# Kernel optimization log

Hardware: AMD Instinct MI355X
Metric: run time of the kernel (lower is better)

The kernel has to match this reference:

```python
import jax, jax.numpy as jnp
import numpy as np

D_MODEL = 1024
N_LAYERS = 4
D_INNER = 2 * D_MODEL          # expand=2
D_STATE = 16
D_CONV = 4
DT_RANK = D_MODEL // 16        # ceil(1024/16)=64
B, T = 2, 1024


def setup_inputs() -> dict:
    key = jax.random.key(0)
    ks = jax.random.split(key, 8)
    s = 0.02
    return {
        "x": jax.random.normal(ks[0], (B, T, D_MODEL), jnp.float32),
        "in_proj_w": jax.random.normal(ks[1], (N_LAYERS, 2 * D_INNER, D_MODEL), jnp.float32) * s,
        "conv_w": jax.random.normal(ks[2], (N_LAYERS, D_INNER, D_CONV), jnp.float32) * s,
        "conv_b": jnp.zeros((N_LAYERS, D_INNER), jnp.float32),
        "x_proj_w": jax.random.normal(ks[3], (N_LAYERS, DT_RANK + 2 * D_STATE, D_INNER), jnp.float32) * s,
        "dt_proj_w": jax.random.normal(ks[4], (N_LAYERS, D_INNER, DT_RANK), jnp.float32) * s,
        "dt_proj_b": jax.random.normal(ks[5], (N_LAYERS, D_INNER), jnp.float32) * 0.1,
        "A_log": jnp.tile(jnp.log(jnp.arange(1.0, D_STATE + 1.0, dtype=jnp.float32)), (N_LAYERS, D_INNER, 1)),
        "Dd": jnp.ones((N_LAYERS, D_INNER), jnp.float32),
        "out_proj_w": jax.random.normal(ks[6], (N_LAYERS, D_MODEL, D_INNER), jnp.float32) * s,
        "norm_w": jnp.ones((D_MODEL,), jnp.float32),
        "norm_b": jnp.zeros((D_MODEL,), jnp.float32),
    }


def _silu(v):
    return v * jax.nn.sigmoid(v)


def _mamba_block(x, in_w, cw, cb, xp_w, dtp_w, dtp_b, A_log, Dv, out_w):
    # x: [B,T,d_model]
    xz = jnp.einsum('btd,ed->bte', x, in_w)            # [B,T,2*d_inner]
    u, z = jnp.split(xz, 2, axis=-1)                   # each [B,T,d_inner]
    # causal depthwise conv over time
    uc = jax.lax.conv_general_dilated(
        u.transpose(0, 2, 1),                          # [B,d_inner,T]
        cw[:, None, :],                                # [d_inner,1,K]
        window_strides=(1,), padding=[(D_CONV - 1, 0)],
        feature_group_count=D_INNER,
        dimension_numbers=('NCH', 'OIH', 'NCH'))
    uc = _silu(uc.transpose(0, 2, 1) + cb)             # [B,T,d_inner]
    x_dbl = jnp.einsum('btd,ed->bte', uc, xp_w)        # [B,T,dt_rank+2*d_state]
    dt_r = x_dbl[..., :DT_RANK]
    Bm = x_dbl[..., DT_RANK:DT_RANK + D_STATE]         # [B,T,d_state]
    Cm = x_dbl[..., DT_RANK + D_STATE:]                # [B,T,d_state]
    dt = jax.nn.softplus(jnp.einsum('btr,dr->btd', dt_r, dtp_w) + dtp_b)  # [B,T,d_inner]
    A = -jnp.exp(A_log)                                # [d_inner,d_state]

    def step(h, inp):
        u_t, dt_t, B_t, C_t = inp                      # [B,dI],[B,dI],[B,dS],[B,dS]
        h = jnp.exp(dt_t[..., None] * A) * h + (dt_t * u_t)[..., None] * B_t[:, None, :]
        return h, jnp.einsum('bds,bs->bd', h, C_t)

    h0 = jnp.zeros((x.shape[0], D_INNER, D_STATE), x.dtype)
    xs = (uc.transpose(1, 0, 2), dt.transpose(1, 0, 2), Bm.transpose(1, 0, 2), Cm.transpose(1, 0, 2))
    _, ys = jax.lax.scan(step, h0, xs)                 # ys: [T,B,d_inner]
    y = ys.transpose(1, 0, 2) + uc * Dv                # skip term D*u
    y = y * _silu(z)                                   # gated
    return jnp.einsum('btd,ed->bte', y, out_w)         # [B,T,d_model]


def reference(x, in_proj_w, conv_w, conv_b, x_proj_w, dt_proj_w, dt_proj_b, A_log, Dd, out_proj_w, norm_w, norm_b):
    for i in range(in_proj_w.shape[0]):
        residual = x
        x = _mamba_block(x, in_proj_w[i], conv_w[i], conv_b[i], x_proj_w[i],
                         dt_proj_w[i], dt_proj_b[i], A_log[i], Dd[i], out_proj_w[i])
        x = x + residual
    mu = jnp.mean(x, -1, keepdims=True)
    var = jnp.var(x, -1, keepdims=True)
    return (x - mu) / jnp.sqrt(var + 1e-5) * norm_w + norm_b
```

## Files before the change

### kernel.cpp

```cpp
#include <hip/hip_runtime.h>
#include <hip/hip_bf16.h>

#define N_LAYERS 4
#define D_MODEL  1024
#define D_INNER  2048
#define D_STATE  16
#define D_CONV   4
#define DT_RANK  64
#define BB       2
#define TT       1024
#define BT       (BB*TT)

#define NCHUNK 16
#define SCTC   (TT/NCHUNK)

#define XP_KS  8

typedef unsigned short ushort_t;
typedef __attribute__((ext_vector_type(8))) short short8;
typedef __attribute__((ext_vector_type(4))) float f32x4;

__device__ __forceinline__ float sigmoidf_(float x){ return 1.f/(1.f+__expf(-x)); }
__device__ __forceinline__ float siluf_(float x){ return x*sigmoidf_(x); }
__device__ __forceinline__ float softplusf_(float x){ return fmaxf(x,0.f) + log1pf(__expf(-fabsf(x))); }
__device__ __forceinline__ ushort_t f2b(float f){
    unsigned int x = __builtin_bit_cast(unsigned int, f);
    unsigned int r = (x + 0x7fffu + ((x>>16)&1u)) >> 16;
    return (ushort_t)r;
}
__device__ __forceinline__ float b2f(ushort_t u){
    unsigned int x = ((unsigned int)u) << 16;
    return __builtin_bit_cast(float, x);
}

#define GLOAD(g, l) __builtin_amdgcn_global_load_lds( \
    (const __attribute__((address_space(1))) void*)(g), \
    (__attribute__((address_space(3))) void*)(l), 16, 0, 0)

__global__ __launch_bounds__(256) void f2b_k(const float* __restrict__ in,
                                             ushort_t* __restrict__ out, int n){
    int i = blockIdx.x*256 + threadIdx.x;
    float4 v = ((const float4*)in)[i];
    ushort4 o;
    o.x = f2b(v.x); o.y = f2b(v.y); o.z = f2b(v.z); o.w = f2b(v.w);
    ((ushort4*)out)[i] = o;
}

__global__ __launch_bounds__(256) void f2b2_k(
    const float* __restrict__ a, ushort_t* __restrict__ ao, int na4,
    const float* __restrict__ b, ushort_t* __restrict__ bo){
    int i = blockIdx.x*256 + threadIdx.x;
    const float4* src; ushort4* dst; int j;
    if (i < na4){ src = (const float4*)a; dst = (ushort4*)ao; j = i; }
    else        { src = (const float4*)b; dst = (ushort4*)bo; j = i - na4; }
    float4 v = src[j];
    ushort4 o;
    o.x = f2b(v.x); o.y = f2b(v.y); o.z = f2b(v.z); o.w = f2b(v.w);
    dst[j] = o;
}

__global__ __launch_bounds__(512) void gemm_ip(
    const ushort_t* __restrict__ A, const ushort_t* __restrict__ W,
    int M, int N, int K, ushort_t* __restrict__ outb,
    int RM, int RN, int XN)
{
    __shared__ ushort_t As[4][128*32];
    __shared__ ushort_t Ws[4][128*32];
    const int tid  = threadIdx.x;
    const int lane = tid & 63;
    const int wv   = tid >> 6;
    const int wm0  = (wv>>2)*64, wn0 = (wv&3)*32;

    const int bid = blockIdx.x;
    const int xcd = bid & 7, bi = bid >> 3;
    const int xm = xcd / XN, xn = xcd - xm*XN;
    const int m0 = (xm*RM + bi/RN)*128;
    const int n0 = (xn*RN + bi - (bi/RN)*RN)*128;

    const int r0 = tid>>2, ch = tid&3;

    f32x4 acc[4][2];
    #pragma unroll
    for (int i=0;i<4;++i)
        #pragma unroll
        for (int j=0;j<2;++j) acc[i][j] = (f32x4){0.f,0.f,0.f,0.f};

    const int row_a = lane & 15, kc = (lane>>4)*8;
    const ushort_t* gA = A + (size_t)(m0+r0)*K + ch*8;
    const ushort_t* gW = W + (size_t)(n0+r0)*K + ch*8;

#define STAGE(KT, BUF) { \
    GLOAD(gA + (KT)*32, (char*)&As[BUF][0] + tid*16); \
    GLOAD(gW + (KT)*32, (char*)&Ws[BUF][0] + tid*16); }

#define COMPUTE(BUF) { \
    short8 af[4], bf[2]; \
    _Pragma("unroll") \
    for (int i=0;i<4;++i) af[i] = *(const short8*)&As[BUF][(wm0 + i*16 + row_a)*32 + kc]; \
    _Pragma("unroll") \
    for (int j=0;j<2;++j) bf[j] = *(const short8*)&Ws[BUF][(wn0 + j*16 + row_a)*32 + kc]; \
    _Pragma("unroll") \
    for (int i=0;i<4;++i) \
        _Pragma("unroll") \
        for (int j=0;j<2;++j) \
            acc[i][j] = __builtin_amdgcn_mfma_f32_16x16x32_bf16(af[i], bf[j], acc[i][j], 0,0,0); }

    const int nt = K >> 5;
    STAGE(0, 0); STAGE(1, 1); STAGE(2, 2);
    for (int t = 0; t < nt-3; ++t){
        asm volatile("s_waitcnt vmcnt(4)" ::: "memory");
        asm volatile("s_barrier" ::: "memory");
        STAGE(t+3, (t+3)&3);
        COMPUTE(t&3);
    }
    asm volatile("s_waitcnt vmcnt(4)" ::: "memory");
    asm volatile("s_barrier" ::: "memory");
    COMPUTE((nt-3)&3);
    asm volatile("s_waitcnt vmcnt(2)" ::: "memory");
    asm volatile("s_barrier" ::: "memory");
    COMPUTE((nt-2)&3);
    asm volatile("s_waitcnt vmcnt(0)" ::: "memory");
    asm volatile("s_barrier" ::: "memory");
    COMPUTE((nt-1)&3);
#undef STAGE
#undef COMPUTE

    const int crow = (lane>>4)*4, ccol = lane & 15;
    #pragma unroll
    for (int i=0;i<4;++i){
        #pragma unroll
        for (int j=0;j<2;++j){
            #pragma unroll
            for (int r=0;r<4;++r){
                int m = m0 + wm0 + i*16 + crow + r;
                int n = n0 + wn0 + j*16 + ccol;
                outb[(size_t)m*N + n] = f2b(acc[i][j][r]);
            }
        }
    }
}

__global__ __launch_bounds__(256) void gemm_op(
    const ushort_t* __restrict__ A, const ushort_t* __restrict__ W,
    float* __restrict__ C, int M, int N, int K,
    const float* __restrict__ res, ushort_t* __restrict__ outb,
    int RM, int RN, int XN)
{
    __shared__ ushort_t As[4][64*32];
    __shared__ ushort_t Ws[4][64*32];
    const int tid  = threadIdx.x;
    const int lane = tid & 63;
    const int wv   = tid >> 6;
    const int wm0  = (wv>>1)*32, wn0 = (wv&1)*32;

    const int bid = blockIdx.x;
    const int xcd = bid & 7, bi = bid >> 3;
    const int xm = xcd / XN, xn = xcd - xm*XN;
    const int m0 = (xm*RM + bi/RN)*64;
    const int n0 = (xn*RN + bi - (bi/RN)*RN)*64;

    const int r0 = tid>>2, ch = tid&3;

    f32x4 acc[2][2];
    #pragma unroll
    for (int i=0;i<2;++i)
        #pragma unroll
        for (int j=0;j<2;++j) acc[i][j] = (f32x4){0.f,0.f,0.f,0.f};

    const int row_a = lane & 15, kc = (lane>>4)*8;
    const ushort_t* gA = A + (size_t)(m0+r0)*K + ch*8;
    const ushort_t* gW = W + (size_t)(n0+r0)*K + ch*8;

#define STAGE(KT, BUF) { \
    GLOAD(gA + (KT)*32, (char*)&As[BUF][0] + tid*16); \
    GLOAD(gW + (KT)*32, (char*)&Ws[BUF][0] + tid*16); }

#define COMPUTE(BUF) { \
    short8 af[2], bf[2]; \
    _Pragma("unroll") \
    for (int i=0;i<2;++i) af[i] = *(const short8*)&As[BUF][(wm0 + i*16 + row_a)*32 + kc]; \
    _Pragma("unroll") \
    for (int j=0;j<2;++j) bf[j] = *(const short8*)&Ws[BUF][(wn0 + j*16 + row_a)*32 + kc]; \
    _Pragma("unroll") \
    for (int i=0;i<2;++i) \
        _Pragma("unroll") \
        for (int j=0;j<2;++j) \
            acc[i][j] = __builtin_amdgcn_mfma_f32_16x16x32_bf16(af[i], bf[j], acc[i][j], 0,0,0); }

    const int nt = K >> 5;
    STAGE(0, 0); STAGE(1, 1); STAGE(2, 2);
    for (int t = 0; t < nt-3; ++t){
        asm volatile("s_waitcnt vmcnt(4)" ::: "memory");
        asm volatile("s_barrier" ::: "memory");
        STAGE(t+3, (t+3)&3);
        COMPUTE(t&3);
    }
    asm volatile("s_waitcnt vmcnt(4)" ::: "memory");
    asm volatile("s_barrier" ::: "memory");
    COMPUTE((nt-3)&3);
    asm volatile("s_waitcnt vmcnt(2)" ::: "memory");
    asm volatile("s_barrier" ::: "memory");
    COMPUTE((nt-2)&3);
    asm volatile("s_waitcnt vmcnt(0)" ::: "memory");
    asm volatile("s_barrier" ::: "memory");
    COMPUTE((nt-1)&3);
#undef STAGE
#undef COMPUTE

    const int crow = (lane>>4)*4, ccol = lane & 15;
    #pragma unroll
    for (int i=0;i<2;++i){
        #pragma unroll
        for (int j=0;j<2;++j){
            #pragma unroll
            for (int r=0;r<4;++r){
                int m = m0 + wm0 + i*16 + crow + r;
                int n = n0 + wn0 + j*16 + ccol;
                float v = acc[i][j][r] + res[(size_t)m*N + n];
                C[(size_t)m*N + n] = v;
                outb[(size_t)m*N + n] = f2b(v);
            }
        }
    }
}

template<int EPI>
__global__ __launch_bounds__(256) void gemm_tn(
    const float* __restrict__ A, int lda,
    const float* __restrict__ W, int ldw,
    float* __restrict__ C, int ldc,
    int M, int N, int K,
    const float* __restrict__ bias)
{
    __shared__ float As[16][68];
    __shared__ float Ws[16][68];
    const int tid = threadIdx.x;
    const int tx = tid & 15, ty = tid >> 4;
    const int m0 = blockIdx.y * 64, n0 = blockIdx.x * 64;
    const int lr = tid >> 2;
    const int lk = (tid & 3) << 2;
    float acc[4][4] = {{0.f}};

    for (int k0 = 0; k0 < K; k0 += 16) {
        float4 av = *(const float4*)(A + (size_t)(m0+lr)*lda + k0 + lk);
        float4 wv = make_float4(0.f,0.f,0.f,0.f);
        if (n0 + lr < N) wv = *(const float4*)(W + (size_t)(n0+lr)*ldw + k0 + lk);
        __syncthreads();
        As[lk+0][lr]=av.x; As[lk+1][lr]=av.y; As[lk+2][lr]=av.z; As[lk+3][lr]=av.w;
        Ws[lk+0][lr]=wv.x; Ws[lk+1][lr]=wv.y; Ws[lk+2][lr]=wv.z; Ws[lk+3][lr]=wv.w;
        __syncthreads();
        #pragma unroll
        for (int k = 0; k < 16; ++k) {
            float4 a = *(const float4*)&As[k][ty<<2];
            float4 b = *(const float4*)&Ws[k][tx<<2];
            float a4[4] = {a.x,a.y,a.z,a.w};
            float b4[4] = {b.x,b.y,b.z,b.w};
            #pragma unroll
            for (int i=0;i<4;++i)
                #pragma unroll
                for (int j=0;j<4;++j)
                    acc[i][j] = fmaf(a4[i], b4[j], acc[i][j]);
        }
    }

    #pragma unroll
    for (int i=0;i<4;++i){
        int m = m0 + (ty<<2) + i;
        #pragma unroll
        for (int j=0;j<4;++j){
            int n = n0 + (tx<<2) + j;
            if (n < N){
                float v = acc[i][j];
                if (EPI==1) v = softplusf_(v + bias[n]);
                C[(size_t)m*ldc + n] = v;
            }
        }
    }
}

__global__ __launch_bounds__(256) void gemm_tn_sk(
    const float* __restrict__ A, int lda,
    const float* __restrict__ W, int ldw,
    float* __restrict__ P, int M, int N, int K)
{
    __shared__ float As[16][68];
    __shared__ float Ws[16][68];
    const int tid = threadIdx.x;
    const int tx = tid & 15, ty = tid >> 4;
    const int m0 = blockIdx.y * 64, n0 = blockIdx.x * 64;
    const int kbase = blockIdx.z * (K/XP_KS);
    const int lr = tid >> 2;
    const int lk = (tid & 3) << 2;
    float acc[4][4] = {{0.f}};

    for (int kk = 0; kk < K/XP_KS; kk += 16) {
        int k0 = kbase + kk;
        float4 av = *(const float4*)(A + (size_t)(m0+lr)*lda + k0 + lk);
        float4 wv = make_float4(0.f,0.f,0.f,0.f);
        if (n0 + lr < N) wv = *(const float4*)(W + (size_t)(n0+lr)*ldw + k0 + lk);
        __syncthreads();
        As[lk+0][lr]=av.x; As[lk+1][lr]=av.y; As[lk+2][lr]=av.z; As[lk+3][lr]=av.w;
        Ws[lk+0][lr]=wv.x; Ws[lk+1][lr]=wv.y; Ws[lk+2][lr]=wv.z; Ws[lk+3][lr]=wv.w;
        __syncthreads();
        #pragma unroll
        for (int k = 0; k < 16; ++k) {
            float4 a = *(const float4*)&As[k][ty<<2];
            float4 b = *(const float4*)&Ws[k][tx<<2];
            float a4[4] = {a.x,a.y,a.z,a.w};
            float b4[4] = {b.x,b.y,b.z,b.w};
            #pragma unroll
            for (int i=0;i<4;++i)
                #pragma unroll
                for (int j=0;j<4;++j)
                    acc[i][j] = fmaf(a4[i], b4[j], acc[i][j]);
        }
    }

    float* Pz = P + (size_t)blockIdx.z * M * 96;
    #pragma unroll
    for (int i=0;i<4;++i){
        int m = m0 + (ty<<2) + i;
        #pragma unroll
        for (int j=0;j<4;++j){
            int n = n0 + (tx<<2) + j;
            if (n < N) Pz[(size_t)m*96 + n] = acc[i][j];
        }
    }
}

__global__ __launch_bounds__(256) void sk_reduce(
    const float* __restrict__ P, float* __restrict__ outp, int MN)
{
    int g = blockIdx.x*256 + threadIdx.x;
    float s = 0.f;
    #pragma unroll
    for (int ks=0; ks<XP_KS; ++ks) s += P[(size_t)ks*MN + g];
    outp[g] = s;
}

__global__ __launch_bounds__(256) void conv_silu_k(
    const ushort_t* __restrict__ xzb, const float* __restrict__ cw,
    const float* __restrict__ cb, float* __restrict__ uc)
{
    int idx = blockIdx.x*256 + threadIdx.x;
    int d  = idx & (D_INNER-1);
    int bt = idx >> 11;
    int t  = bt & (TT-1);
    float4 w4 = *(const float4*)(cw + d*4);
    float wv[4] = {w4.x, w4.y, w4.z, w4.w};
    float acc = cb[d];
    #pragma unroll
    for (int k=0;k<4;++k){
        int tt = t - 3 + k;
        if (tt >= 0) acc = fmaf(b2f(xzb[(size_t)(bt-3+k)*4096 + d]), wv[k], acc);
    }
    uc[idx] = siluf_(acc);
}


__global__ __launch_bounds__(256) void scan_p1(
    const float* __restrict__ dt, const float* __restrict__ uc,
    const float* __restrict__ xdbl, const float* __restrict__ A_log,
    float* __restrict__ hpart, float* __restrict__ hdecay)
{
    const int tid = threadIdx.x;
    const int d = blockIdx.x*256 + tid;
    const int b = blockIdx.y;
    const int k = blockIdx.z;
    const int t0 = k*SCTC;
    float A[16];
    #pragma unroll
    for (int q=0;q<4;++q){
        float4 v = *(const float4*)(A_log + (size_t)d*16 + q*4);
        A[q*4+0]=-__expf(v.x); A[q*4+1]=-__expf(v.y);
        A[q*4+2]=-__expf(v.z); A[q*4+3]=-__expf(v.w);
    }
    float h[16];
    #pragma unroll
    for (int s=0;s<16;++s) h[s]=0.f;
    float sumdt = 0.f;
    const float* dtp = dt + ((size_t)b*TT + t0)*D_INNER + d;
    const float* ucp = uc + ((size_t)b*TT + t0)*D_INNER + d;
    const float* bcp = xdbl + ((size_t)b*TT + t0)*96 + 64;
    #pragma unroll 2
    for (int t=0;t<SCTC;++t){
        float dtv = dtp[(size_t)t*D_INNER];
        float uv  = ucp[(size_t)t*D_INNER];
        const float* bc = bcp + (size_t)t*96;
        float du = dtv*uv;
        sumdt += dtv;
        #pragma unroll
        for (int s=0;s<16;++s)
            h[s] = fmaf(__expf(dtv*A[s]), h[s], du*bc[s]);
    }
    size_t base = ((size_t)(k*BB+b)*D_INNER + d)*16;
    float4* hp = (float4*)(hpart + base);
    float4* hd = (float4*)(hdecay + base);
    #pragma unroll
    for (int q=0;q<4;++q){
        hp[q] = make_float4(h[q*4],h[q*4+1],h[q*4+2],h[q*4+3]);
        hd[q] = make_float4(__expf(sumdt*A[q*4+0]),__expf(sumdt*A[q*4+1]),
                            __expf(sumdt*A[q*4+2]),__expf(sumdt*A[q*4+3]));
    }
}

__global__ __launch_bounds__(256) void scan_fix(
    const float* __restrict__ hpart, const float* __restrict__ hdecay,
    float* __restrict__ hstart)
{
    int g = blockIdx.x*256 + threadIdx.x;
    float h = 0.f;
    #pragma unroll
    for (int k=0;k<NCHUNK;++k){
        size_t idx = (size_t)k*(BB*D_INNER*16) + g;
        hstart[idx] = h;
        h = fmaf(hdecay[idx], h, hpart[idx]);
    }
}

__global__ __launch_bounds__(256) void scan_p3(
    const float* __restrict__ dt, const float* __restrict__ uc,
    const float* __restrict__ xdbl, const float* __restrict__ A_log,
    const ushort_t* __restrict__ xzb, const float* __restrict__ Dd,
    const float* __restrict__ hstart, ushort_t* __restrict__ ysb)
{
    const int tid = threadIdx.x;
    const int d = blockIdx.x*256 + tid;
    const int b = blockIdx.y;
    const int k = blockIdx.z;
    const int t0 = k*SCTC;
    float A[16];
    #pragma unroll
    for (int q=0;q<4;++q){
        float4 v = *(const float4*)(A_log + (size_t)d*16 + q*4);
        A[q*4+0]=-__expf(v.x); A[q*4+1]=-__expf(v.y);
        A[q*4+2]=-__expf(v.z); A[q*4+3]=-__expf(v.w);
    }
    float h[16];
    {
        const float4* hs = (const float4*)(hstart + ((size_t)(k*BB+b)*D_INNER + d)*16);
        #pragma unroll
        for (int q=0;q<4;++q){
            float4 v = hs[q];
            h[q*4+0]=v.x; h[q*4+1]=v.y; h[q*4+2]=v.z; h[q*4+3]=v.w;
        }
    }
    const float Ddc = Dd[d];
    const float* dtp = dt + ((size_t)b*TT + t0)*D_INNER + d;
    const float* ucp = uc + ((size_t)b*TT + t0)*D_INNER + d;
    const ushort_t* zp = xzb + ((size_t)b*TT + t0)*4096 + 2048 + d;
    const float* bcp = xdbl + ((size_t)b*TT + t0)*96 + 64;
    ushort_t* yp = ysb + ((size_t)b*TT + t0)*D_INNER + d;
    #pragma unroll 2
    for (int t=0;t<SCTC;++t){
        float dtv = dtp[(size_t)t*D_INNER];
        float uv  = ucp[(size_t)t*D_INNER];
        float zv  = b2f(zp[(size_t)t*4096]);
        const float* bc = bcp + (size_t)t*96;
        float du = dtv*uv;
        float y0=0.f,y1=0.f,y2=0.f,y3=0.f;
        #pragma unroll
        for (int q=0;q<4;++q){
            h[q*4+0] = fmaf(__expf(dtv*A[q*4+0]), h[q*4+0], du*bc[q*4+0]);
            h[q*4+1] = fmaf(__expf(dtv*A[q*4+1]), h[q*4+1], du*bc[q*4+1]);
            h[q*4+2] = fmaf(__expf(dtv*A[q*4+2]), h[q*4+2], du*bc[q*4+2]);
            h[q*4+3] = fmaf(__expf(dtv*A[q*4+3]), h[q*4+3], du*bc[q*4+3]);
        }
        #pragma unroll
        for (int q=0;q<4;++q){
            y0 = fmaf(h[q*4+0], bc[16+q*4+0], y0);
            y1 = fmaf(h[q*4+1], bc[16+q*4+1], y1);
            y2 = fmaf(h[q*4+2], bc[16+q*4+2], y2);
            y3 = fmaf(h[q*4+3], bc[16+q*4+3], y3);
        }
        float y = (y0+y1)+(y2+y3);
        float yv = (y + uv*Ddc) * siluf_(zv);
        yp[(size_t)t*D_INNER] = f2b(yv);
    }
}

__global__ __launch_bounds__(256) void layernorm_k(
    const float* __restrict__ X, const float* __restrict__ w,
    const float* __restrict__ b, float* __restrict__ out)
{
    int row = blockIdx.x;
    int tid = threadIdx.x;
    const float* xr = X + (size_t)row*D_MODEL;
    float4 v = *(const float4*)(xr + tid*4);
    float s  = v.x+v.y+v.z+v.w;
    float ss = fmaf(v.x,v.x, fmaf(v.y,v.y, fmaf(v.z,v.z, v.w*v.w)));
    #pragma unroll
    for (int off=32; off>0; off>>=1){
        s  += __shfl_down(s, off, 64);
        ss += __shfl_down(ss, off, 64);
    }
    __shared__ float red[8];
    int wid = tid>>6, lane = tid&63;
    if (lane==0){ red[wid]=s; red[4+wid]=ss; }
    __syncthreads();
    if (tid==0){
        float S  = red[0]+red[1]+red[2]+red[3];
        float SS = red[4]+red[5]+red[6]+red[7];
        float mu = S*(1.f/D_MODEL);
        float var = SS*(1.f/D_MODEL) - mu*mu;
        red[0]=mu; red[1]=rsqrtf(var + 1e-5f);
    }
    __syncthreads();
    float mu=red[0], rs=red[1];
    float4 wv = *(const float4*)(w + tid*4);
    float4 bv = *(const float4*)(b + tid*4);
    float4 o;
    o.x = fmaf((v.x-mu)*rs, wv.x, bv.x);
    o.y = fmaf((v.y-mu)*rs, wv.y, bv.y);
    o.z = fmaf((v.z-mu)*rs, wv.z, bv.z);
    o.w = fmaf((v.w-mu)*rs, wv.w, bv.w);
    *(float4*)(out + (size_t)row*D_MODEL + tid*4) = o;
}

extern "C" void kernel_launch(void* const* d_in, const int* in_sizes, int n_in,
                              void* d_out, int out_size, void* d_ws, size_t ws_size,
                              hipStream_t stream) {
    (void)in_sizes; (void)n_in; (void)out_size; (void)ws_size;
    const float* x      = (const float*)d_in[0];
    const float* in_w   = (const float*)d_in[1];
    const float* conv_w = (const float*)d_in[2];
    const float* conv_b = (const float*)d_in[3];
    const float* xp_w   = (const float*)d_in[4];
    const float* dtp_w  = (const float*)d_in[5];
    const float* dtp_b  = (const float*)d_in[6];
    const float* A_log  = (const float*)d_in[7];
    const float* Dd     = (const float*)d_in[8];
    const float* out_w  = (const float*)d_in[9];
    const float* nw     = (const float*)d_in[10];
    const float* nb     = (const float*)d_in[11];
    float* out = (float*)d_out;

    char* p = (char*)d_ws;
    ushort_t* xzb  = (ushort_t*)p; p += (size_t)BT*4096*2;
    float* uc      = (float*)p;  p += (size_t)BT*2048*4;
    float* xdbl    = (float*)p;  p += (size_t)BT*96*4;
    float* dtb     = (float*)p;  p += (size_t)BT*2048*4;
    float* xcur    = (float*)p;  p += (size_t)BT*1024*4;
    ushort_t* xinb = (ushort_t*)p; p += (size_t)BT*1024*2;
    ushort_t* ysb  = (ushort_t*)p; p += (size_t)BT*2048*2;
    ushort_t* winb = (ushort_t*)p; p += (size_t)4096*1024*2;
    ushort_t* woutb= (ushort_t*)p; p += (size_t)1024*2048*2;

    float* pbuf   = (float*)winb;
    float* hpart  = (float*)winb;
    float* hdecay = hpart + (size_t)NCHUNK*BB*D_INNER*16;
    float* hstart = (float*)xinb;

    f2b_k<<<(BT*1024)/1024,256,0,stream>>>(x, xinb, BT*1024);

    for (int i = 0; i < N_LAYERS; ++i){
        const float* xin = (i==0) ? x : xcur;
        f2b2_k<<<(4096*1024 + 1024*2048)/1024,256,0,stream>>>(
            in_w + (size_t)i*4096*D_MODEL, winb, (4096*1024)/4,
            out_w + (size_t)i*D_MODEL*D_INNER, woutb);
        gemm_ip<<<512,512,0,stream>>>(
            xinb, winb, BT, 4096, D_MODEL, xzb, 8, 8, 4);
        conv_silu_k<<<(BT*D_INNER)/256,256,0,stream>>>(
            xzb, conv_w + (size_t)i*D_INNER*D_CONV, conv_b + (size_t)i*D_INNER, uc);
        gemm_tn_sk<<<dim3(2,32,XP_KS),256,0,stream>>>(
            uc, D_INNER, xp_w + (size_t)i*96*D_INNER, D_INNER,
            pbuf, BT, 96, D_INNER);
        sk_reduce<<<(BT*96)/256,256,0,stream>>>(pbuf, xdbl, BT*96);
        gemm_tn<1><<<dim3(32,32),256,0,stream>>>(
            xdbl, 96, dtp_w + (size_t)i*D_INNER*DT_RANK, DT_RANK,
            dtb, D_INNER, BT, D_INNER, DT_RANK, dtp_b + (size_t)i*D_INNER);
        scan_p1<<<dim3(D_INNER/256, BB, NCHUNK),256,0,stream>>>(
            dtb, uc, xdbl, A_log + (size_t)i*D_INNER*D_STATE, hpart, hdecay);
        scan_fix<<<(BB*D_INNER*16)/256,256,0,stream>>>(hpart, hdecay, hstart);
        scan_p3<<<dim3(D_INNER/256, BB, NCHUNK),256,0,stream>>>(
            dtb, uc, xdbl, A_log + (size_t)i*D_INNER*D_STATE, xzb,
            Dd + (size_t)i*D_INNER, hstart, ysb);
        gemm_op<<<512,256,0,stream>>>(
            ysb, woutb, xcur, BT, 1024, D_INNER, xin, xinb, 8, 8, 2);
    }
    layernorm_k<<<BT,256,0,stream>>>(xcur, nw, nb, out);
}
```

Measured before the change: 753.1 us.

## Store uc and dt in bf16, MFMA dt_proj, hoist weight conversion, more scan chunks

```diff
diff --git a/kernel.cpp b/kernel.cpp
--- a/kernel.cpp
+++ b/kernel.cpp
@@ -11,7 +11,7 @@
 #define TT       1024
 #define BT       (BB*TT)
 
-#define NCHUNK 16
+#define NCHUNK 32
 #define SCTC   (TT/NCHUNK)
 
 #define XP_KS  8
@@ -46,13 +46,18 @@
     ((ushort4*)out)[i] = o;
 }
 
-__global__ __launch_bounds__(256) void f2b2_k(
-    const float* __restrict__ a, ushort_t* __restrict__ ao, int na4,
-    const float* __restrict__ b, ushort_t* __restrict__ bo){
+__global__ __launch_bounds__(256) void f2bw_k(
+    const float* __restrict__ in_w, const float* __restrict__ out_w,
+    const float* __restrict__ dtp_w,
+    ushort_t* __restrict__ winb, ushort_t* __restrict__ woutb,
+    ushort_t* __restrict__ dtpb){
+    const int n1 = (N_LAYERS*4096*1024)/4;
+    const int n2 = (N_LAYERS*1024*2048)/4;
     int i = blockIdx.x*256 + threadIdx.x;
     const float4* src; ushort4* dst; int j;
-    if (i < na4){ src = (const float4*)a; dst = (ushort4*)ao; j = i; }
-    else        { src = (const float4*)b; dst = (ushort4*)bo; j = i - na4; }
+    if (i < n1){ src=(const float4*)in_w;  dst=(ushort4*)winb;  j=i; }
+    else if (i < n1+n2){ src=(const float4*)out_w; dst=(ushort4*)woutb; j=i-n1; }
+    else { src=(const float4*)dtp_w; dst=(ushort4*)dtpb; j=i-n1-n2; }
     float4 v = src[j];
     ushort4 o;
     o.x = f2b(v.x); o.y = f2b(v.y); o.z = f2b(v.z); o.w = f2b(v.w);
@@ -224,29 +229,85 @@
     }
 }
 
-template<int EPI>
-__global__ __launch_bounds__(256) void gemm_tn(
-    const float* __restrict__ A, int lda,
+__global__ __launch_bounds__(256) void dt_mfma(
+    const ushort_t* __restrict__ A, const ushort_t* __restrict__ W,
+    const float* __restrict__ bias, ushort_t* __restrict__ dtb, int N)
+{
+    __shared__ ushort_t As[2][64*32];
+    __shared__ ushort_t Ws[2][64*32];
+    const int tid = threadIdx.x, lane = tid&63, wv = tid>>6;
+    const int wm0 = (wv>>1)*32, wn0 = (wv&1)*32;
+    const int m0 = blockIdx.y*64, n0 = blockIdx.x*64;
+    const int r0 = tid>>2, ch = tid&3;
+    const ushort_t* gA = A + (size_t)(m0+r0)*64 + ch*8;
+    const ushort_t* gW = W + (size_t)(n0+r0)*64 + ch*8;
+    GLOAD(gA,      (char*)&As[0][0] + tid*16);
+    GLOAD(gW,      (char*)&Ws[0][0] + tid*16);
+    GLOAD(gA + 32, (char*)&As[1][0] + tid*16);
+    GLOAD(gW + 32, (char*)&Ws[1][0] + tid*16);
+
+    f32x4 acc[2][2];
+    #pragma unroll
+    for (int i=0;i<2;++i)
+        #pragma unroll
+        for (int j=0;j<2;++j) acc[i][j] = (f32x4){0.f,0.f,0.f,0.f};
+
+    asm volatile("s_waitcnt vmcnt(0)" ::: "memory");
+    asm volatile("s_barrier" ::: "memory");
+    const int row_a = lane&15, kc = (lane>>4)*8;
+    #pragma unroll
+    for (int buf=0; buf<2; ++buf){
+        short8 af[2], bf[2];
+        #pragma unroll
+        for (int i=0;i<2;++i) af[i] = *(const short8*)&As[buf][(wm0 + i*16 + row_a)*32 + kc];
+        #pragma unroll
+        for (int j=0;j<2;++j) bf[j] = *(const short8*)&Ws[buf][(wn0 + j*16 + row_a)*32 + kc];
+        #pragma unroll
+        for (int i=0;i<2;++i)
+            #pragma unroll
+            for (int j=0;j<2;++j)
+                acc[i][j] = __builtin_amdgcn_mfma_f32_16x16x32_bf16(af[i], bf[j], acc[i][j], 0,0,0);
+    }
+
+    const int crow = (lane>>4)*4, ccol = lane & 15;
+    #pragma unroll
+    for (int i=0;i<2;++i){
+        #pragma unroll
+        for (int j=0;j<2;++j){
+            #pragma unroll
+            for (int r=0;r<4;++r){
+                int m = m0 + wm0 + i*16 + crow + r;
+                int n = n0 + wn0 + j*16 + ccol;
+                float v = softplusf_(acc[i][j][r] + bias[n]);
+                dtb[(size_t)m*N + n] = f2b(v);
+            }
+        }
+    }
+}
+
+__global__ __launch_bounds__(256) void gemm_tn_sk(
+    const ushort_t* __restrict__ A, int lda,
     const float* __restrict__ W, int ldw,
-    float* __restrict__ C, int ldc,
-    int M, int N, int K,
-    const float* __restrict__ bias)
+    float* __restrict__ P, int M, int N, int K)
 {
     __shared__ float As[16][68];
     __shared__ float Ws[16][68];
     const int tid = threadIdx.x;
     const int tx = tid & 15, ty = tid >> 4;
     const int m0 = blockIdx.y * 64, n0 = blockIdx.x * 64;
+    const int kbase = blockIdx.z * (K/XP_KS);
     const int lr = tid >> 2;
     const int lk = (tid & 3) << 2;
     float acc[4][4] = {{0.f}};
 
-    for (int k0 = 0; k0 < K; k0 += 16) {
-        float4 av = *(const float4*)(A + (size_t)(m0+lr)*lda + k0 + lk);
+    for (int kk = 0; kk < K/XP_KS; kk += 16) {
+        int k0 = kbase + kk;
+        ushort4 av4 = *(const ushort4*)(A + (size_t)(m0+lr)*lda + k0 + lk);
         float4 wv = make_float4(0.f,0.f,0.f,0.f);
         if (n0 + lr < N) wv = *(const float4*)(W + (size_t)(n0+lr)*ldw + k0 + lk);
         __syncthreads();
-        As[lk+0][lr]=av.x; As[lk+1][lr]=av.y; As[lk+2][lr]=av.z; As[lk+3][lr]=av.w;
+        As[lk+0][lr]=b2f(av4.x); As[lk+1][lr]=b2f(av4.y);
+        As[lk+2][lr]=b2f(av4.z); As[lk+3][lr]=b2f(av4.w);
         Ws[lk+0][lr]=wv.x; Ws[lk+1][lr]=wv.y; Ws[lk+2][lr]=wv.z; Ws[lk+3][lr]=wv.w;
         __syncthreads();
         #pragma unroll
@@ -263,59 +324,6 @@
         }
     }
 
-    #pragma unroll
-    for (int i=0;i<4;++i){
-        int m = m0 + (ty<<2) + i;
-        #pragma unroll
-        for (int j=0;j<4;++j){
-            int n = n0 + (tx<<2) + j;
-            if (n < N){
-                float v = acc[i][j];
-                if (EPI==1) v = softplusf_(v + bias[n]);
-                C[(size_t)m*ldc + n] = v;
-            }
-        }
-    }
-}
-
-__global__ __launch_bounds__(256) void gemm_tn_sk(
-    const float* __restrict__ A, int lda,
-    const float* __restrict__ W, int ldw,
-    float* __restrict__ P, int M, int N, int K)
-{
-    __shared__ float As[16][68];
-    __shared__ float Ws[16][68];
-    const int tid = threadIdx.x;
-    const int tx = tid & 15, ty = tid >> 4;
-    const int m0 = blockIdx.y * 64, n0 = blockIdx.x * 64;
-    const int kbase = blockIdx.z * (K/XP_KS);
-    const int lr = tid >> 2;
-    const int lk = (tid & 3) << 2;
-    float acc[4][4] = {{0.f}};
-
-    for (int kk = 0; kk < K/XP_KS; kk += 16) {
-        int k0 = kbase + kk;
-        float4 av = *(const float4*)(A + (size_t)(m0+lr)*lda + k0 + lk);
-        float4 wv = make_float4(0.f,0.f,0.f,0.f);
-        if (n0 + lr < N) wv = *(const float4*)(W + (size_t)(n0+lr)*ldw + k0 + lk);
-        __syncthreads();
-        As[lk+0][lr]=av.x; As[lk+1][lr]=av.y; As[lk+2][lr]=av.z; As[lk+3][lr]=av.w;
-        Ws[lk+0][lr]=wv.x; Ws[lk+1][lr]=wv.y; Ws[lk+2][lr]=wv.z; Ws[lk+3][lr]=wv.w;
-        __syncthreads();
-        #pragma unroll
-        for (int k = 0; k < 16; ++k) {
-            float4 a = *(const float4*)&As[k][ty<<2];
-            float4 b = *(const float4*)&Ws[k][tx<<2];
-            float a4[4] = {a.x,a.y,a.z,a.w};
-            float b4[4] = {b.x,b.y,b.z,b.w};
-            #pragma unroll
-            for (int i=0;i<4;++i)
-                #pragma unroll
-                for (int j=0;j<4;++j)
-                    acc[i][j] = fmaf(a4[i], b4[j], acc[i][j]);
-        }
-    }
-
     float* Pz = P + (size_t)blockIdx.z * M * 96;
     #pragma unroll
     for (int i=0;i<4;++i){
@@ -329,18 +337,21 @@
 }
 
 __global__ __launch_bounds__(256) void sk_reduce(
-    const float* __restrict__ P, float* __restrict__ outp, int MN)
+    const float* __restrict__ P, float* __restrict__ outp,
+    ushort_t* __restrict__ dtrb, int MN)
 {
     int g = blockIdx.x*256 + threadIdx.x;
     float s = 0.f;
     #pragma unroll
     for (int ks=0; ks<XP_KS; ++ks) s += P[(size_t)ks*MN + g];
     outp[g] = s;
+    int m = g / 96, c = g - m*96;
+    if (c < 64) dtrb[(size_t)m*64 + c] = f2b(s);
 }
 
 __global__ __launch_bounds__(256) void conv_silu_k(
     const ushort_t* __restrict__ xzb, const float* __restrict__ cw,
-    const float* __restrict__ cb, float* __restrict__ uc)
+    const float* __restrict__ cb, ushort_t* __restrict__ ucb)
 {
     int idx = blockIdx.x*256 + threadIdx.x;
     int d  = idx & (D_INNER-1);
@@ -354,12 +365,12 @@
         int tt = t - 3 + k;
         if (tt >= 0) acc = fmaf(b2f(xzb[(size_t)(bt-3+k)*4096 + d]), wv[k], acc);
     }
-    uc[idx] = siluf_(acc);
+    ucb[idx] = f2b(siluf_(acc));
 }
 
 
 __global__ __launch_bounds__(256) void scan_p1(
-    const float* __restrict__ dt, const float* __restrict__ uc,
+    const ushort_t* __restrict__ dt, const ushort_t* __restrict__ uc,
     const float* __restrict__ xdbl, const float* __restrict__ A_log,
     float* __restrict__ hpart, float* __restrict__ hdecay)
 {
@@ -379,13 +390,13 @@
     #pragma unroll
     for (int s=0;s<16;++s) h[s]=0.f;
     float sumdt = 0.f;
-    const float* dtp = dt + ((size_t)b*TT + t0)*D_INNER + d;
-    const float* ucp = uc + ((size_t)b*TT + t0)*D_INNER + d;
+    const ushort_t* dtp = dt + ((size_t)b*TT + t0)*D_INNER + d;
+    const ushort_t* ucp = uc + ((size_t)b*TT + t0)*D_INNER + d;
     const float* bcp = xdbl + ((size_t)b*TT + t0)*96 + 64;
     #pragma unroll 2
     for (int t=0;t<SCTC;++t){
-        float dtv = dtp[(size_t)t*D_INNER];
-        float uv  = ucp[(size_t)t*D_INNER];
+        float dtv = b2f(dtp[(size_t)t*D_INNER]);
+        float uv  = b2f(ucp[(size_t)t*D_INNER]);
         const float* bc = bcp + (size_t)t*96;
         float du = dtv*uv;
         sumdt += dtv;
@@ -419,7 +430,7 @@
 }
 
 __global__ __launch_bounds__(256) void scan_p3(
-    const float* __restrict__ dt, const float* __restrict__ uc,
+    const ushort_t* __restrict__ dt, const ushort_t* __restrict__ uc,
     const float* __restrict__ xdbl, const float* __restrict__ A_log,
     const ushort_t* __restrict__ xzb, const float* __restrict__ Dd,
     const float* __restrict__ hstart, ushort_t* __restrict__ ysb)
@@ -446,15 +457,15 @@
         }
     }
     const float Ddc = Dd[d];
-    const float* dtp = dt + ((size_t)b*TT + t0)*D_INNER + d;
-    const float* ucp = uc + ((size_t)b*TT + t0)*D_INNER + d;
+    const ushort_t* dtp = dt + ((size_t)b*TT + t0)*D_INNER + d;
+    const ushort_t* ucp = uc + ((size_t)b*TT + t0)*D_INNER + d;
     const ushort_t* zp = xzb + ((size_t)b*TT + t0)*4096 + 2048 + d;
     const float* bcp = xdbl + ((size_t)b*TT + t0)*96 + 64;
     ushort_t* yp = ysb + ((size_t)b*TT + t0)*D_INNER + d;
     #pragma unroll 2
     for (int t=0;t<SCTC;++t){
-        float dtv = dtp[(size_t)t*D_INNER];
-        float uv  = ucp[(size_t)t*D_INNER];
+        float dtv = b2f(dtp[(size_t)t*D_INNER]);
+        float uv  = b2f(ucp[(size_t)t*D_INNER]);
         float zv  = b2f(zp[(size_t)t*4096]);
         const float* bc = bcp + (size_t)t*96;
         float du = dtv*uv;
@@ -537,46 +548,46 @@
 
     char* p = (char*)d_ws;
     ushort_t* xzb  = (ushort_t*)p; p += (size_t)BT*4096*2;
-    float* uc      = (float*)p;  p += (size_t)BT*2048*4;
+    ushort_t* ucb  = (ushort_t*)p; p += (size_t)BT*2048*2;
     float* xdbl    = (float*)p;  p += (size_t)BT*96*4;
-    float* dtb     = (float*)p;  p += (size_t)BT*2048*4;
+    ushort_t* dtrb = (ushort_t*)p; p += (size_t)BT*64*2;
+    ushort_t* dtbb = (ushort_t*)p; p += (size_t)BT*2048*2;
     float* xcur    = (float*)p;  p += (size_t)BT*1024*4;
     ushort_t* xinb = (ushort_t*)p; p += (size_t)BT*1024*2;
     ushort_t* ysb  = (ushort_t*)p; p += (size_t)BT*2048*2;
-    ushort_t* winb = (ushort_t*)p; p += (size_t)4096*1024*2;
-    ushort_t* woutb= (ushort_t*)p; p += (size_t)1024*2048*2;
-
-    float* pbuf   = (float*)winb;
-    float* hpart  = (float*)winb;
-    float* hdecay = hpart + (size_t)NCHUNK*BB*D_INNER*16;
-    float* hstart = (float*)xinb;
+    ushort_t* winb = (ushort_t*)p; p += (size_t)N_LAYERS*4096*1024*2;
+    ushort_t* woutb= (ushort_t*)p; p += (size_t)N_LAYERS*1024*2048*2;
+    ushort_t* dtpb = (ushort_t*)p; p += (size_t)N_LAYERS*2048*64*2;
+    float* hpart   = (float*)p;  p += (size_t)NCHUNK*BB*D_INNER*16*4;
+    float* hdecay  = (float*)p;  p += (size_t)NCHUNK*BB*D_INNER*16*4;
+    float* hstart  = (float*)p;  p += (size_t)NCHUNK*BB*D_INNER*16*4;
+    float* pbuf    = hpart;
 
     f2b_k<<<(BT*1024)/1024,256,0,stream>>>(x, xinb, BT*1024);
+    f2bw_k<<<(N_LAYERS*(4096*1024 + 1024*2048 + 2048*64))/1024,256,0,stream>>>(
+        in_w, out_w, dtp_w, winb, woutb, dtpb);
 
     for (int i = 0; i < N_LAYERS; ++i){
         const float* xin = (i==0) ? x : xcur;
-        f2b2_k<<<(4096*1024 + 1024*2048)/1024,256,0,stream>>>(
-            in_w + (size_t)i*4096*D_MODEL, winb, (4096*1024)/4,
-            out_w + (size_t)i*D_MODEL*D_INNER, woutb);
         gemm_ip<<<512,512,0,stream>>>(
-            xinb, winb, BT, 4096, D_MODEL, xzb, 8, 8, 4);
+            xinb, winb + (size_t)i*4096*1024, BT, 4096, D_MODEL, xzb, 8, 8, 4);
         conv_silu_k<<<(BT*D_INNER)/256,256,0,stream>>>(
-            xzb, conv_w + (size_t)i*D_INNER*D_CONV, conv_b + (size_t)i*D_INNER, uc);
+            xzb, conv_w + (size_t)i*D_INNER*D_CONV, conv_b + (size_t)i*D_INNER, ucb);
         gemm_tn_sk<<<dim3(2,32,XP_KS),256,0,stream>>>(
-            uc, D_INNER, xp_w + (size_t)i*96*D_INNER, D_INNER,
+            ucb, D_INNER, xp_w + (size_t)i*96*D_INNER, D_INNER,
             pbuf, BT, 96, D_INNER);
-        sk_reduce<<<(BT*96)/256,256,0,stream>>>(pbuf, xdbl, BT*96);
-        gemm_tn<1><<<dim3(32,32),256,0,stream>>>(
-            xdbl, 96, dtp_w + (size_t)i*D_INNER*DT_RANK, DT_RANK,
-            dtb, D_INNER, BT, D_INNER, DT_RANK, dtp_b + (size_t)i*D_INNER);
+        sk_reduce<<<(BT*96)/256,256,0,stream>>>(pbuf, xdbl, dtrb, BT*96);
+        dt_mfma<<<dim3(D_INNER/64, BT/64),256,0,stream>>>(
+            dtrb, dtpb + (size_t)i*2048*64, dtp_b + (size_t)i*D_INNER, dtbb, D_INNER);
         scan_p1<<<dim3(D_INNER/256, BB, NCHUNK),256,0,stream>>>(
-            dtb, uc, xdbl, A_log + (size_t)i*D_INNER*D_STATE, hpart, hdecay);
+            dtbb, ucb, xdbl, A_log + (size_t)i*D_INNER*D_STATE, hpart, hdecay);
         scan_fix<<<(BB*D_INNER*16)/256,256,0,stream>>>(hpart, hdecay, hstart);
         scan_p3<<<dim3(D_INNER/256, BB, NCHUNK),256,0,stream>>>(
-            dtb, uc, xdbl, A_log + (size_t)i*D_INNER*D_STATE, xzb,
+            dtbb, ucb, xdbl, A_log + (size_t)i*D_INNER*D_STATE, xzb,
             Dd + (size_t)i*D_INNER, hstart, ysb);
         gemm_op<<<512,256,0,stream>>>(
-            ysb, woutb, xcur, BT, 1024, D_INNER, xin, xinb, 8, 8, 2);
+            ysb, woutb + (size_t)i*1024*2048, xcur, BT, 1024, D_INNER,
+            xin, xinb, 8, 8, 2);
     }
     layernorm_k<<<BT,256,0,stream>>>(xcur, nw, nb, out);
 }
```

New measurement: 681.6 us. -9.5%, faster.
